# Optimization experiments

Hardware: AMD Instinct MI355X
Metric: run time of the kernel (lower is better)

Reference implementation:

```python
import jax, jax.numpy as jnp
import numpy as np

N_CAM, N_PTS, N_OBS = 2000, 500000, 5000000


def setup_inputs() -> dict:
    key = jax.random.key(0)
    k1, k2, k3, k4, k5, k6 = jax.random.split(key, 6)
    # SE3 poses: [tx, ty, tz, qx, qy, qz, qw] (pypose layout), unit quaternions
    t = jax.random.normal(k1, (N_CAM, 3), dtype=jnp.float32) * 5.0
    t = t.at[:, 2].set(jax.random.uniform(k2, (N_CAM,), minval=100.0, maxval=200.0))
    q = jax.random.normal(k3, (N_CAM, 4), dtype=jnp.float32)
    q = q / jnp.linalg.norm(q, axis=-1, keepdims=True)
    poses = jnp.concatenate([t, q], axis=-1)  # [N_CAM, 7]
    points = jax.random.normal(k4, (N_PTS, 3), dtype=jnp.float32) * 5.0  # [N_PTS, 3]
    # Pinhole intrinsics
    K = jnp.array([[1000.0, 0.0, 640.0], [0.0, 1000.0, 360.0], [0.0, 0.0, 1.0]], dtype=jnp.float32)
    observes = jax.random.normal(k5, (N_OBS, 2), dtype=jnp.float32) * 100.0 + 500.0
    ki, kj = jax.random.split(k6)
    cidx = jax.random.randint(ki, (N_OBS,), 0, N_CAM, dtype=jnp.int64)
    pidx = jax.random.randint(kj, (N_OBS,), 0, N_PTS, dtype=jnp.int64)
    return {"observes": observes, "K": K, "poses": poses, "points": points, "cidx": cidx, "pidx": pidx}


def _se3_act(pose7, pts):
    # pose7: [N,7] (t, q) with q=(x,y,z,w); pts: [N,3]
    t = pose7[:, :3]
    qv = pose7[:, 3:6]
    qw = pose7[:, 6:7]
    # p' = p + 2 * qv x (qv x p + w p) + t   (unit-quaternion rotation)
    uv = jnp.cross(qv, pts)
    return pts + 2.0 * jnp.cross(qv, uv + qw * pts) + t


def reference(observes, K, poses, points, cidx, pidx):
    p_cam = _se3_act(poses[cidx], points[pidx])  # [N_OBS, 3] camera-frame points
    img = p_cam @ K.T                            # [N_OBS, 3] homogeneous pixels
    projs = img[:, :2] / img[:, 2:3]             # [N_OBS, 2]
    return (projs - observes).reshape(-1)        # [N_OBS * 2]
```

## Files before the change

### kernel.cpp

```cpp
#include <hip/hip_runtime.h>


typedef float vfloat4 __attribute__((ext_vector_type(4)));
typedef int   vint4   __attribute__((ext_vector_type(4)));

__global__ __launch_bounds__(256) void pad_points(
    const float* __restrict__ src, vfloat4* __restrict__ dst, int n_pts)
{
    int i = blockIdx.x * blockDim.x + threadIdx.x;
    if (i >= n_pts) return;
    const float* s = src + 3 * i;
    vfloat4 v = {s[0], s[1], s[2], 0.0f};
    dst[i] = v;
}

__global__ __launch_bounds__(256) void pad_poses(
    const float* __restrict__ src, vfloat4* __restrict__ dst, int n_cam)
{
    int i = blockIdx.x * blockDim.x + threadIdx.x;
    if (i >= n_cam) return;
    const float* s = src + 7 * i;
    vfloat4 a = {s[0], s[1], s[2], s[3]};
    vfloat4 b = {s[4], s[5], s[6], 0.0f};
    dst[2 * i]     = a;
    dst[2 * i + 1] = b;
}

__global__ __launch_bounds__(256) void resid_kernel4p(
    const float*   __restrict__ obs,
    const float*   __restrict__ Kmat,
    const vfloat4* __restrict__ poses_pad,
    const vfloat4* __restrict__ points_pad,
    const int*     __restrict__ cidx,
    const int*     __restrict__ pidx,
    float*         __restrict__ out,
    int n)
{
    int t = blockIdx.x * blockDim.x + threadIdx.x;
    int base = t * 4;

    float fx = Kmat[0], cx = Kmat[2];
    float fy = Kmat[4], cy = Kmat[5];

    if (base + 4 <= n) {
        vint4   c4  = __builtin_nontemporal_load((const vint4*)(cidx + base));
        vint4   p4  = __builtin_nontemporal_load((const vint4*)(pidx + base));
        vfloat4 o01 = __builtin_nontemporal_load((const vfloat4*)(obs + 2 * base));
        vfloat4 o23 = __builtin_nontemporal_load((const vfloat4*)(obs + 2 * base + 4));

        int cc[4] = {c4.x, c4.y, c4.z, c4.w};
        int pp[4] = {p4.x, p4.y, p4.z, p4.w};

        vfloat4 P[4], QA[4], QB[4];
        #pragma unroll
        for (int k = 0; k < 4; ++k) P[k] = points_pad[pp[k]];
        #pragma unroll
        for (int k = 0; k < 4; ++k) {
            QA[k] = poses_pad[2 * cc[k]];
            QB[k] = poses_pad[2 * cc[k] + 1];
        }

        float res[8];
        #pragma unroll
        for (int k = 0; k < 4; ++k) {
            float px = P[k].x, py = P[k].y, pz = P[k].z;
            float tx = QA[k].x, ty = QA[k].y, tz = QA[k].z;
            float qx = QA[k].w, qy = QB[k].x, qz = QB[k].y, qw = QB[k].z;

            float ux = qy * pz - qz * py;
            float uy = qz * px - qx * pz;
            float uz = qx * py - qy * px;
            float wx = ux + qw * px;
            float wy = uy + qw * py;
            float wz = uz + qw * pz;
            float ccx = qy * wz - qz * wy;
            float ccy = qz * wx - qx * wz;
            float ccz = qx * wy - qy * wx;
            float X = px + 2.0f * ccx + tx;
            float Y = py + 2.0f * ccy + ty;
            float Z = pz + 2.0f * ccz + tz;

            float invz = 1.0f / Z;
            res[2 * k]     = fx * X * invz + cx;
            res[2 * k + 1] = fy * Y * invz + cy;
        }

        vfloat4 r0 = {res[0] - o01.x, res[1] - o01.y, res[2] - o01.z, res[3] - o01.w};
        vfloat4 r1 = {res[4] - o23.x, res[5] - o23.y, res[6] - o23.z, res[7] - o23.w};
        __builtin_nontemporal_store(r0, (vfloat4*)(out + 2 * base));
        __builtin_nontemporal_store(r1, (vfloat4*)(out + 2 * base + 4));
    } else {
        for (int i = base; i < n; ++i) {
            vfloat4 P  = points_pad[pidx[i]];
            vfloat4 QA = poses_pad[2 * cidx[i]];
            vfloat4 QB = poses_pad[2 * cidx[i] + 1];
            float px = P.x, py = P.y, pz = P.z;
            float tx = QA.x, ty = QA.y, tz = QA.z;
            float qx = QA.w, qy = QB.x, qz = QB.y, qw = QB.z;

            float ux = qy * pz - qz * py;
            float uy = qz * px - qx * pz;
            float uz = qx * py - qy * px;
            float wx = ux + qw * px;
            float wy = uy + qw * py;
            float wz = uz + qw * pz;
            float ccx = qy * wz - qz * wy;
            float ccy = qz * wx - qx * wz;
            float ccz = qx * wy - qy * wx;
            float X = px + 2.0f * ccx + tx;
            float Y = py + 2.0f * ccy + ty;
            float Z = pz + 2.0f * ccz + tz;

            float invz = 1.0f / Z;
            out[2 * i]     = fx * X * invz + cx - obs[2 * i];
            out[2 * i + 1] = fy * Y * invz + cy - obs[2 * i + 1];
        }
    }
}

__global__ __launch_bounds__(256) void resid_fallback(
    const float* __restrict__ obs, const float* __restrict__ Kmat,
    const float* __restrict__ poses, const float* __restrict__ points,
    const int* __restrict__ cidx, const int* __restrict__ pidx,
    float* __restrict__ out, int n)
{
    int i = blockIdx.x * blockDim.x + threadIdx.x;
    if (i >= n) return;
    const float* ps = poses + 7 * cidx[i];
    const float* pt = points + 3 * pidx[i];
    float px = pt[0], py = pt[1], pz = pt[2];
    float tx = ps[0], ty = ps[1], tz = ps[2];
    float qx = ps[3], qy = ps[4], qz = ps[5], qw = ps[6];
    float ux = qy * pz - qz * py;
    float uy = qz * px - qx * pz;
    float uz = qx * py - qy * px;
    float wx = ux + qw * px;
    float wy = uy + qw * py;
    float wz = uz + qw * pz;
    float ccx = qy * wz - qz * wy;
    float ccy = qz * wx - qx * wz;
    float ccz = qx * wy - qy * wx;
    float X = px + 2.0f * ccx + tx;
    float Y = py + 2.0f * ccy + ty;
    float Z = pz + 2.0f * ccz + tz;
    float invz = 1.0f / Z;
    out[2 * i]     = Kmat[0] * X * invz + Kmat[2] - obs[2 * i];
    out[2 * i + 1] = Kmat[4] * Y * invz + Kmat[5] - obs[2 * i + 1];
}

extern "C" void kernel_launch(void* const* d_in, const int* in_sizes, int n_in,
                              void* d_out, int out_size, void* d_ws, size_t ws_size,
                              hipStream_t stream) {
    const float* obs    = (const float*)d_in[0];
    const float* Kmat   = (const float*)d_in[1];
    const float* poses  = (const float*)d_in[2];
    const float* points = (const float*)d_in[3];
    const int*   cidx   = (const int*)d_in[4];
    const int*   pidx   = (const int*)d_in[5];
    float*       out    = (float*)d_out;

    int n     = in_sizes[4];
    int n_cam = in_sizes[2] / 7;
    int n_pts = in_sizes[3] / 3;

    size_t pts_bytes  = (size_t)n_pts * 16;
    size_t pose_bytes = (size_t)n_cam * 32;

    if (ws_size < pts_bytes + pose_bytes) {
        resid_fallback<<<(n + 255) / 256, 256, 0, stream>>>(
            obs, Kmat, poses, points, cidx, pidx, out, n);
        return;
    }

    vfloat4* points_pad = (vfloat4*)d_ws;
    vfloat4* poses_pad  = (vfloat4*)((char*)d_ws + pts_bytes);

    pad_points<<<(n_pts + 255) / 256, 256, 0, stream>>>(points, points_pad, n_pts);
    pad_poses<<<(n_cam + 255) / 256, 256, 0, stream>>>(poses, poses_pad, n_cam);

    int per_block = 256 * 4;
    int grid = (n + per_block - 1) / per_block;
    resid_kernel4p<<<grid, 256, 0, stream>>>(
        obs, Kmat, poses_pad, points_pad, cidx, pidx, out, n);
}
```

Before: 188.5 us.

## Stage padded camera poses in LDS per block and use 1024-thread blocks

Each block now copies the whole padded pose table (2000 cameras, 64 KB) into shared memory, then reads camera poses from LDS instead of global memory. The block size goes from 256 to 1024 threads to spread that preload over more observations. The goal is to take the random pose gathers off the L2/global path. In exchange, every one of about 1221 blocks reloads 64 KB and waits at a barrier, and the large LDS footprint limits occupancy to about one block per CU. Runs with more than 2000 cameras fall back to the slow kernel.

```diff
diff --git a/kernel.cpp b/kernel.cpp
--- a/kernel.cpp
+++ b/kernel.cpp
@@ -3,6 +3,8 @@
 
 typedef float vfloat4 __attribute__((ext_vector_type(4)));
 typedef int   vint4   __attribute__((ext_vector_type(4)));
+
+#define MAX_CAM 2000
 
 __global__ __launch_bounds__(256) void pad_points(
     const float* __restrict__ src, vfloat4* __restrict__ dst, int n_pts)
@@ -26,7 +28,7 @@
     dst[2 * i + 1] = b;
 }
 
-__global__ __launch_bounds__(256) void resid_kernel4p(
+__global__ __launch_bounds__(1024) void resid_lds(
     const float*   __restrict__ obs,
     const float*   __restrict__ Kmat,
     const vfloat4* __restrict__ poses_pad,
@@ -34,8 +36,15 @@
     const int*     __restrict__ cidx,
     const int*     __restrict__ pidx,
     float*         __restrict__ out,
-    int n)
+    int n, int n_cam)
 {
+    __shared__ vfloat4 sposes[2 * MAX_CAM];
+
+    int rows = 2 * n_cam;
+    for (int r = threadIdx.x; r < rows; r += blockDim.x)
+        sposes[r] = poses_pad[r];
+    __syncthreads();
+
     int t = blockIdx.x * blockDim.x + threadIdx.x;
     int base = t * 4;
 
@@ -51,13 +60,15 @@
         int cc[4] = {c4.x, c4.y, c4.z, c4.w};
         int pp[4] = {p4.x, p4.y, p4.z, p4.w};
 
-        vfloat4 P[4], QA[4], QB[4];
+        vfloat4 P[4];
         #pragma unroll
         for (int k = 0; k < 4; ++k) P[k] = points_pad[pp[k]];
+
+        vfloat4 QA[4], QB[4];
         #pragma unroll
         for (int k = 0; k < 4; ++k) {
-            QA[k] = poses_pad[2 * cc[k]];
-            QB[k] = poses_pad[2 * cc[k] + 1];
+            QA[k] = sposes[2 * cc[k]];
+            QB[k] = sposes[2 * cc[k] + 1];
         }
 
         float res[8];
@@ -92,8 +103,8 @@
     } else {
         for (int i = base; i < n; ++i) {
             vfloat4 P  = points_pad[pidx[i]];
-            vfloat4 QA = poses_pad[2 * cidx[i]];
-            vfloat4 QB = poses_pad[2 * cidx[i] + 1];
+            vfloat4 QA = sposes[2 * cidx[i]];
+            vfloat4 QB = sposes[2 * cidx[i] + 1];
             float px = P.x, py = P.y, pz = P.z;
             float tx = QA.x, ty = QA.y, tz = QA.z;
             float qx = QA.w, qy = QB.x, qz = QB.y, qw = QB.z;
@@ -166,7 +177,7 @@
     size_t pts_bytes  = (size_t)n_pts * 16;
     size_t pose_bytes = (size_t)n_cam * 32;
 
-    if (ws_size < pts_bytes + pose_bytes) {
+    if (ws_size < pts_bytes + pose_bytes || n_cam > MAX_CAM) {
         resid_fallback<<<(n + 255) / 256, 256, 0, stream>>>(
             obs, Kmat, poses, points, cidx, pidx, out, n);
         return;
@@ -178,8 +189,9 @@
     pad_points<<<(n_pts + 255) / 256, 256, 0, stream>>>(points, points_pad, n_pts);
     pad_poses<<<(n_cam + 255) / 256, 256, 0, stream>>>(poses, poses_pad, n_cam);
 
-    int per_block = 256 * 4;
+    int block = 1024;
+    int per_block = block * 4;
     int grid = (n + per_block - 1) / per_block;
-    resid_kernel4p<<<grid, 256, 0, stream>>>(
-        obs, Kmat, poses_pad, points_pad, cidx, pidx, out, n);
+    resid_lds<<<grid, block, 0, stream>>>(
+        obs, Kmat, poses_pad, points_pad, cidx, pidx, out, n, n_cam);
 }
```

Measured after the change: 179.6 us. 1.05x faster.
